# Performance work log

Measured on AMD Instinct MI355X. Metric: run time of the kernel, lower is better.

The kernel has to match this reference:

```python
import jax, jax.numpy as jnp
import numpy as np

B, C, H, W = 16, 256, 32, 32
N_E, E_DIM = 8192, 256
BETA = 0.25
ENT_RATIO = 0.1
TEMP = 0.01


def _normalize(x, eps=1e-6):
    # torch F.normalize: x / clamp_min(||x||, eps)
    n = jnp.linalg.norm(x, axis=-1, keepdims=True)
    return x / jnp.maximum(n, eps)


def setup_inputs() -> dict:
    key = jax.random.key(0)
    k1, k2, k3 = jax.random.split(key, 3)
    z = jax.random.normal(k1, (B, C, H, W), dtype=jnp.float32)
    # nn.Embedding init: normal(0, e_dim**-0.5)
    emb_weight = jax.random.normal(k2, (N_E, E_DIM), dtype=jnp.float32) * (E_DIM ** -0.5)
    # nn.Linear(e_dim, e_dim)
    proj_w = jax.random.normal(k3, (E_DIM, E_DIM), dtype=jnp.float32) * (E_DIM ** -0.5)
    proj_b = jnp.zeros((E_DIM,), dtype=jnp.float32)
    return {"z": z, "emb_weight": emb_weight, "proj_w": proj_w, "proj_b": proj_b}


def reference(z, emb_weight, proj_w, proj_b):
    sg = jax.lax.stop_gradient
    # SimVQ: project the (frozen) codebook through a linear layer
    weight = emb_weight @ proj_w.T + proj_b            # [K, d]
    b, c, h, w = z.shape
    z_bhwc = jnp.transpose(z, (0, 2, 3, 1))            # [B,H,W,C]
    z_flat = z_bhwc.reshape(b, h * w, c)               # [B,L,C]

    # l2_norm=True branch
    zn = _normalize(z_flat)                             # [B,L,d]
    wn = _normalize(weight)                             # [K,d]

    z2 = jnp.sum(zn * zn, axis=-1, keepdims=True)       # [B,L,1]
    w2 = jnp.sum(wn * wn, axis=-1)[None, None, :]       # [1,1,K]
    dot = jnp.einsum('bld,kd->blk', zn, wn)             # [B,L,K]
    dists = z2 + w2 - 2.0 * dot                         # [B,L,K]

    indices = jnp.argmin(dists, axis=-1)                # [B,L]
    q = wn[indices].reshape(b, h, w, c)                 # gather normalized codebook

    # training losses (l2_norm=True -> compare normalized)
    z_cmp = _normalize(z_bhwc)
    q_cmp = _normalize(q)
    codebook_loss = jnp.mean((q_cmp - sg(z_cmp)) ** 2)
    commit_loss = BETA * jnp.mean((sg(q_cmp) - z_cmp) ** 2)

    # entropy loss on affinity = -dists
    a = (-dists).reshape(-1, dists.shape[-1]) / TEMP    # [B*L, K]
    probs = jax.nn.softmax(a, axis=-1)
    log_probs = jax.nn.log_softmax(a + 1e-5, axis=-1)
    avg_probs = jnp.mean(probs, axis=0)
    avg_entropy = -jnp.sum(avg_probs * jnp.log(avg_probs + 1e-5))
    sample_entropy = -jnp.mean(jnp.sum(probs * log_probs, axis=-1))
    entropy_loss = ENT_RATIO * (sample_entropy - avg_entropy)

    # straight-through estimator, back to channel-first
    z_q = z_bhwc + sg(q - z_bhwc)
    z_q = jnp.transpose(z_q, (0, 3, 1, 2))              # [B,C,H,W]
    flat_indices = indices.reshape(-1)
    return (z_q, codebook_loss, commit_loss, entropy_loss, flat_indices)
```

## Files before the change

### kernel.cpp

```cpp
#include <hip/hip_runtime.h>
#include <math.h>

#define NROWS 16384
#define NCODES 8192
#define DIMS 256
#define NCS 4
#define CEXP 288.5390082f

#define OFF_WN   0u
#define OFF_W2   2097152u
#define OFF_ZN   2105344u
#define OFF_WNH  6299648u
#define OFF_WNL  7348224u
#define OFF_ZNH  8396800u
#define OFF_ZNL  10493952u
#define OFF_PL1  12591104u
#define OFF_PL2  12656640u
#define OFF_PS   12722176u
#define OFF_PI1  12787712u
#define OFF_PI2  12853248u
#define OFF_RM   12918784u
#define OFF_RS   12935168u
#define OFF_RIDX 12951552u
#define OFF_AVGP 12967936u
#define OFF_SCAL 12976128u

typedef __attribute__((ext_vector_type(8))) short bf16x8;
typedef __attribute__((ext_vector_type(4))) float f32x4;
typedef unsigned short u16;

__device__ __forceinline__ u16 f2bf(float f) {
  unsigned u = __float_as_uint(f);
  u += 0x7fffu + ((u >> 16) & 1u);
  return (u16)(u >> 16);
}
__device__ __forceinline__ float bf2f(u16 s) { return __uint_as_float(((unsigned)s) << 16); }

__device__ __forceinline__ void gl_lds16(const u16* g, u16* l) {
  __builtin_amdgcn_global_load_lds(
      (const __attribute__((address_space(1))) unsigned*)g,
      (__attribute__((address_space(3))) unsigned*)l, 16, 0, 0);
}

#define PHASE_BARRIER_CNT()  asm volatile("s_waitcnt vmcnt(2) lgkmcnt(0)\n\ts_barrier" ::: "memory")
#define PHASE_BARRIER_ALL()  asm volatile("s_waitcnt vmcnt(0) lgkmcnt(0)\n\ts_barrier" ::: "memory")
#define LGKM_BARRIER()       asm volatile("s_waitcnt lgkmcnt(0)\n\ts_barrier" ::: "memory")
#define DRAIN_VM()           asm volatile("s_waitcnt vmcnt(0)" ::: "memory")

__device__ __forceinline__ void ins2(float x, int idx, float& b1, int& i1, float& b2, int& i2) {
  if (x > b1 || (x == b1 && idx < i1)) { b2 = b1; i2 = i1; b1 = x; i1 = idx; }
  else if (x > b2 || (x == b2 && idx < i2)) { b2 = x; i2 = idx; }
}

__global__ __launch_bounds__(256) void k0_init(float* ws) {
  int i = blockIdx.x * 256 + threadIdx.x;
  if (i < NCODES) ws[OFF_AVGP + i] = 0.f;
  if (i < 16) ws[OFF_SCAL + i] = 0.f;
}

__global__ __launch_bounds__(256) void k1_codebook(const float* __restrict__ emb,
    const float* __restrict__ pw, const float* __restrict__ pb,
    float* __restrict__ wn, float* __restrict__ w2,
    u16* __restrict__ wnh, u16* __restrict__ wnl) {
  __shared__ float e[256];
  __shared__ float red[256];
  int k = blockIdx.x, t = threadIdx.x;
  e[t] = emb[(size_t)k * 256 + t];
  __syncthreads();
  const float4* prow = reinterpret_cast<const float4*>(pw + (size_t)t * 256);
  float acc = pb[t];
  #pragma unroll 8
  for (int q = 0; q < 64; ++q) {
    float4 p4 = prow[q];
    acc += e[q*4+0]*p4.x + e[q*4+1]*p4.y + e[q*4+2]*p4.z + e[q*4+3]*p4.w;
  }
  red[t] = acc * acc;
  __syncthreads();
  for (int s = 128; s; s >>= 1) { if (t < s) red[t] += red[t+s]; __syncthreads(); }
  float inv = 1.f / fmaxf(sqrtf(red[0]), 1e-6f);
  float v = acc * inv;
  size_t o = (size_t)k*256 + t;
  wn[o] = v;
  u16 hb = f2bf(v); float hf = bf2f(hb);
  wnh[o] = hb; wnl[o] = f2bf(v - hf);
  __syncthreads();
  red[t] = v * v;
  __syncthreads();
  for (int s = 128; s; s >>= 1) { if (t < s) red[t] += red[t+s]; __syncthreads(); }
  if (t == 0) w2[k] = red[0];
}

__global__ __launch_bounds__(256) void k2_zn(const float* __restrict__ z,
    float* __restrict__ zn, u16* __restrict__ znh, u16* __restrict__ znl) {
  __shared__ float tile[256][33];
  __shared__ float inv[32];
  int bh = blockIdx.x, t = threadIdx.x;
  const float* zb = z + (size_t)(bh >> 5) * (256*1024) + (size_t)(bh & 31) * 32;
  for (int j = 0; j < 32; ++j) {
    int i = t + j*256; int c = i >> 5, w = i & 31;
    tile[c][w] = zb[(size_t)c*1024 + w];
  }
  __syncthreads();
  if (t < 32) {
    float s = 0.f;
    for (int c = 0; c < 256; ++c) { float v = tile[c][t]; s += v*v; }
    inv[t] = 1.f / fmaxf(sqrtf(s), 1e-6f);
  }
  __syncthreads();
  size_t base = (size_t)bh * 32 * 256;
  for (int w = 0; w < 32; ++w) {
    float v = tile[t][w] * inv[w];
    size_t o = base + (size_t)w*256 + t;
    zn[o] = v;
    u16 hb = f2bf(v); float hf = bf2f(hb);
    znh[o] = hb; znl[o] = f2bf(v - hf);
  }
}

__global__ __attribute__((amdgpu_flat_work_group_size(512,512)))
__attribute__((amdgpu_waves_per_eu(2,4))) void k3_pass1(
    const u16* __restrict__ znh, const u16* __restrict__ znl,
    const u16* __restrict__ wnh, const u16* __restrict__ wnl,
    float* __restrict__ pL1, float* __restrict__ pL2, float* __restrict__ pS,
    int* __restrict__ pI1, int* __restrict__ pI2) {
  __shared__ u16 Cbuf[3][2][128*32];
  __shared__ float mrgF[4][2][32][3];
  __shared__ int   mrgI[4][2][32][2];
  int t = threadIdx.x;
  int rb = blockIdx.x >> 2, cs = blockIdx.x & 3;
  int r0 = rb * 128;
  int w = t >> 6, l = t & 63;
  int wxc = w & 1, wy = w >> 1;
  int g = l >> 4, lr = l & 15;

  bf16x8 bh[2][8], bl[2][8];
  #pragma unroll
  for (int jr = 0; jr < 2; ++jr) {
    size_t rbase = (size_t)(r0 + wy*32 + jr*16 + lr) * 256;
    #pragma unroll
    for (int dc = 0; dc < 8; ++dc) {
      bh[jr][dc] = *(const bf16x8*)&znh[rbase + dc*32 + g*8];
      bl[jr][dc] = *(const bf16x8*)&znl[rbase + dc*32 + g*8];
    }
  }

  const size_t csbase = (size_t)cs * 2048 * 256;
  auto stage = [&](int s, int b) {
    int dc2 = s & 7;
    int krow = (s >> 3) * 128;
    int code = t >> 2, q = t & 3;
    size_t go = csbase + (size_t)(krow + code)*256 + dc2*32 + q*8;
    gl_lds16(&wnh[go], &Cbuf[b][0][w*512]);
    gl_lds16(&wnl[go], &Cbuf[b][1][w*512]);
  };
  DRAIN_VM();
  stage(0, 0);
  stage(1, 1);

  float b1[2] = {-3.0e38f, -3.0e38f}, b2[2] = {-3.0e38f, -3.0e38f}, Sv[2] = {0.f, 0.f};
  int i1[2] = {0, 0}, i2[2] = {0, 0};

  for (int kt = 0; kt < 16; ++kt) {
    f32x4 acc[4][2];
    #pragma unroll
    for (int i = 0; i < 4; ++i) { acc[i][0] = (f32x4){0.f,0.f,0.f,0.f}; acc[i][1] = (f32x4){0.f,0.f,0.f,0.f}; }
    #pragma unroll
    for (int dc = 0; dc < 8; ++dc) {
      int s = kt*8 + dc;
      if (s < 127) PHASE_BARRIER_CNT(); else PHASE_BARRIER_ALL();
      if (s + 2 < 128) {
        int bS = s + 2; bS -= (bS/3)*3;
        stage(s + 2, bS);
      }
      int bR = s - (s/3)*3;
      #pragma unroll
      for (int i = 0; i < 4; ++i) {
        int co = (wxc*64 + i*16 + lr)*32 + g*8;
        bf16x8 ah = *(const bf16x8*)&Cbuf[bR][0][co];
        bf16x8 al = *(const bf16x8*)&Cbuf[bR][1][co];
        acc[i][0] = __builtin_amdgcn_mfma_f32_16x16x32_bf16(ah, bh[0][dc], acc[i][0], 0, 0, 0);
        acc[i][1] = __builtin_amdgcn_mfma_f32_16x16x32_bf16(ah, bh[1][dc], acc[i][1], 0, 0, 0);
        acc[i][0] = __builtin_amdgcn_mfma_f32_16x16x32_bf16(ah, bl[0][dc], acc[i][0], 0, 0, 0);
        acc[i][1] = __builtin_amdgcn_mfma_f32_16x16x32_bf16(ah, bl[1][dc], acc[i][1], 0, 0, 0);
        acc[i][0] = __builtin_amdgcn_mfma_f32_16x16x32_bf16(al, bh[0][dc], acc[i][0], 0, 0, 0);
        acc[i][1] = __builtin_amdgcn_mfma_f32_16x16x32_bf16(al, bh[1][dc], acc[i][1], 0, 0, 0);
      }
    }
    int kb16 = kt * 16;
    #pragma unroll
    for (int jr = 0; jr < 2; ++jr) {
      float xv[16];
      #pragma unroll
      for (int n = 0; n < 16; ++n) xv[n] = acc[n>>2][jr][n&3];
      float ob1 = b1[jr];
      #pragma unroll
      for (int n = 0; n < 16; ++n) {
        float x = xv[n];
        bool c1 = x > b1[jr];
        bool c2 = x > b2[jr];
        float hi = fmaxf(x, b1[jr]);
        float lo = fminf(x, b1[jr]);
        b2[jr] = fmaxf(lo, fminf(hi, b2[jr]));
        i2[jr] = c1 ? i1[jr] : (c2 ? (kb16 + n) : i2[jr]);
        b1[jr] = hi;
        i1[jr] = c1 ? (kb16 + n) : i1[jr];
      }
      float negCm = -CEXP * b1[jr];
      float ts0 = 0.f, ts1 = 0.f;
      #pragma unroll
      for (int n = 0; n < 16; n += 2) {
        ts0 += exp2f(fmaf(CEXP, xv[n],   negCm));
        ts1 += exp2f(fmaf(CEXP, xv[n+1], negCm));
      }
      Sv[jr] = Sv[jr] * exp2f(CEXP * (ob1 - b1[jr])) + (ts0 + ts1);
    }
  }
  float my[2], y2[2]; int gi1[2], gi2[2];
  #pragma unroll
  for (int jr = 0; jr < 2; ++jr) {
    int e1 = i1[jr], e2 = i2[jr];
    int base = cs*2048 + wxc*64 + g*4;
    gi1[jr] = base + (e1>>4)*128 + ((e1&15)>>2)*16 + (e1&3);
    gi2[jr] = base + (e2>>4)*128 + ((e2&15)>>2)*16 + (e2&3);
    my[jr] = CEXP * b1[jr];
    y2[jr] = CEXP * b2[jr];
    #pragma unroll
    for (int mask = 16; mask <= 32; mask <<= 1) {
      float om  = __shfl_xor(my[jr], mask, 64);
      float oy2 = __shfl_xor(y2[jr], mask, 64);
      float oS  = __shfl_xor(Sv[jr], mask, 64);
      int   o1  = __shfl_xor(gi1[jr], mask, 64);
      int   o2  = __shfl_xor(gi2[jr], mask, 64);
      float pm = my[jr];
      ins2(om,  o1, my[jr], gi1[jr], y2[jr], gi2[jr]);
      ins2(oy2, o2, my[jr], gi1[jr], y2[jr], gi2[jr]);
      Sv[jr] = Sv[jr] * exp2f(pm - my[jr]) + oS * exp2f(om - my[jr]);
    }
  }
  __syncthreads();
  if (g == 0) {
    #pragma unroll
    for (int jr = 0; jr < 2; ++jr) {
      int ri = jr*16 + lr;
      mrgF[wy][wxc][ri][0] = my[jr]; mrgF[wy][wxc][ri][1] = y2[jr]; mrgF[wy][wxc][ri][2] = Sv[jr];
      mrgI[wy][wxc][ri][0] = gi1[jr]; mrgI[wy][wxc][ri][1] = gi2[jr];
    }
  }
  __syncthreads();
  if (t < 128) {
    int wyy = t >> 5, ri = t & 31;
    float m1 = mrgF[wyy][0][ri][0], m2 = mrgF[wyy][0][ri][1], S = mrgF[wyy][0][ri][2];
    int a1 = mrgI[wyy][0][ri][0], a2 = mrgI[wyy][0][ri][1];
    float om1 = mrgF[wyy][1][ri][0], om2 = mrgF[wyy][1][ri][1], oS = mrgF[wyy][1][ri][2];
    int ob1i = mrgI[wyy][1][ri][0], ob2i = mrgI[wyy][1][ri][1];
    float pm = m1;
    ins2(om1, ob1i, m1, a1, m2, a2);
    ins2(om2, ob2i, m1, a1, m2, a2);
    S = S * exp2f(pm - m1) + oS * exp2f(om1 - m1);
    int r = r0 + wyy*32 + ri;
    size_t o = (size_t)cs * NROWS + r;
    pL1[o] = m1; pL2[o] = m2; pS[o] = S;
    pI1[o] = a1; pI2[o] = a2;
  }
}

__global__ __launch_bounds__(256) void k3b_refine(
    const float* __restrict__ zn, const float* __restrict__ wn, const float* __restrict__ w2,
    const float* __restrict__ pL1, const float* __restrict__ pL2, const float* __restrict__ pS,
    const int* __restrict__ pI1, const int* __restrict__ pI2,
    float* __restrict__ rm, float* __restrict__ rs, int* __restrict__ ridx) {
  int t = threadIdx.x;
  int r = blockIdx.x * 4 + (t >> 6);
  int l = t & 63;
  float b1 = pL1[r], b2 = pL2[r], S = pS[r];
  int i1 = pI1[r], i2 = pI2[r];
  #pragma unroll
  for (int c = 1; c < NCS; ++c) {
    size_t o = (size_t)c * NROWS + r;
    float ob1 = pL1[o], ob2 = pL2[o], oS = pS[o];
    int oi1 = pI1[o], oi2 = pI2[o];
    float pb1 = b1;
    ins2(ob1, oi1, b1, i1, b2, i2);
    ins2(ob2, oi2, b1, i1, b2, i2);
    S = S * exp2f(pb1 - b1) + oS * exp2f(ob1 - b1);
  }
  int cand = (l < 32) ? i1 : i2;
  int lo = l & 31;
  const float* zr = zn + (size_t)r * 256;
  const float* wc = wn + (size_t)cand * 256;
  float d = 0.f;
  #pragma unroll
  for (int q = 0; q < 8; ++q) d += zr[lo + q*32] * wc[lo + q*32];
  #pragma unroll
  for (int mask = 1; mask <= 16; mask <<= 1) d += __shfl_xor(d, mask, 64);
  float dOther = __shfl_xor(d, 32, 64);
  if (l == 0) {
    float s1 = w2[i1] - 2.f*d;
    float s2 = w2[i2] - 2.f*dOther;
    int win = i1;
    if (s2 < s1 || (s2 == s1 && i2 < i1)) win = i2;
    rm[r] = b1; rs[r] = S; ridx[r] = win;
  }
}

__global__ __attribute__((amdgpu_flat_work_group_size(512,512)))
__attribute__((amdgpu_waves_per_eu(2,4))) void k4_pass2(
    const u16* __restrict__ znh, const u16* __restrict__ znl,
    const u16* __restrict__ wnh, const u16* __restrict__ wnl,
    const float* __restrict__ rm, const float* __restrict__ rs,
    float* __restrict__ avgp, float* __restrict__ scal) {
  __shared__ u16 Cbuf[3][2][128*32];
  __shared__ float avgLds[4][128];
  __shared__ float red[512];
  int t = threadIdx.x;
  int rb = blockIdx.x >> 2, cs = blockIdx.x & 3;
  int r0 = rb * 128;
  int w = t >> 6, l = t & 63;
  int wxc = w & 1, wy = w >> 1;
  int g = l >> 4, lr = l & 15;

  bf16x8 bh[2][8], bl[2][8];
  #pragma unroll
  for (int jr = 0; jr < 2; ++jr) {
    size_t rbase = (size_t)(r0 + wy*32 + jr*16 + lr) * 256;
    #pragma unroll
    for (int dc = 0; dc < 8; ++dc) {
      bh[jr][dc] = *(const bf16x8*)&znh[rbase + dc*32 + g*8];
      bl[jr][dc] = *(const bf16x8*)&znl[rbase + dc*32 + g*8];
    }
  }
  float m_[2], invS[2], l2s[2];
  #pragma unroll
  for (int jr = 0; jr < 2; ++jr) {
    int r = r0 + wy*32 + jr*16 + lr;
    float mm = rm[r], ss = rs[r];
    m_[jr] = mm; invS[jr] = 1.f / ss; l2s[jr] = log2f(ss);
  }

  const size_t csbase = (size_t)cs * 2048 * 256;
  auto stage = [&](int s, int b) {
    int dc2 = s & 7;
    int krow = (s >> 3) * 128;
    int code = t >> 2, q = t & 3;
    size_t go = csbase + (size_t)(krow + code)*256 + dc2*32 + q*8;
    gl_lds16(&wnh[go], &Cbuf[b][0][w*512]);
    gl_lds16(&wnl[go], &Cbuf[b][1][w*512]);
  };
  DRAIN_VM();
  stage(0, 0);
  stage(1, 1);
  float ent = 0.f;

  for (int kt = 0; kt < 16; ++kt) {
    f32x4 acc[4][2];
    #pragma unroll
    for (int i = 0; i < 4; ++i) { acc[i][0] = (f32x4){0.f,0.f,0.f,0.f}; acc[i][1] = (f32x4){0.f,0.f,0.f,0.f}; }
    #pragma unroll
    for (int dc = 0; dc < 8; ++dc) {
      int s = kt*8 + dc;
      if (s < 127) PHASE_BARRIER_CNT(); else PHASE_BARRIER_ALL();
      if (s + 2 < 128) {
        int bS = s + 2; bS -= (bS/3)*3;
        stage(s + 2, bS);
      }
      int bR = s - (s/3)*3;
      #pragma unroll
      for (int i = 0; i < 4; ++i) {
        int co = (wxc*64 + i*16 + lr)*32 + g*8;
        bf16x8 ah = *(const bf16x8*)&Cbuf[bR][0][co];
        bf16x8 al = *(const bf16x8*)&Cbuf[bR][1][co];
        acc[i][0] = __builtin_amdgcn_mfma_f32_16x16x32_bf16(ah, bh[0][dc], acc[i][0], 0, 0, 0);
        acc[i][1] = __builtin_amdgcn_mfma_f32_16x16x32_bf16(ah, bh[1][dc], acc[i][1], 0, 0, 0);
        acc[i][0] = __builtin_amdgcn_mfma_f32_16x16x32_bf16(ah, bl[0][dc], acc[i][0], 0, 0, 0);
        acc[i][1] = __builtin_amdgcn_mfma_f32_16x16x32_bf16(ah, bl[1][dc], acc[i][1], 0, 0, 0);
        acc[i][0] = __builtin_amdgcn_mfma_f32_16x16x32_bf16(al, bh[0][dc], acc[i][0], 0, 0, 0);
        acc[i][1] = __builtin_amdgcn_mfma_f32_16x16x32_bf16(al, bh[1][dc], acc[i][1], 0, 0, 0);
      }
    }
    int kb = cs*2048 + kt*128;
    float codeAcc[16];
    #pragma unroll
    for (int n = 0; n < 16; ++n) codeAcc[n] = 0.f;
    #pragma unroll
    for (int jr = 0; jr < 2; ++jr) {
      float m = m_[jr], is = invS[jr], l2 = l2s[jr];
      #pragma unroll
      for (int i = 0; i < 4; ++i)
        #pragma unroll
        for (int v = 0; v < 4; ++v) {
          float tt = fmaf(CEXP, acc[i][jr][v], -m);
          float p = exp2f(tt) * is;
          ent -= p * (tt - l2);
          codeAcc[i*4+v] += p;
        }
    }
    #pragma unroll
    for (int n = 0; n < 16; ++n) {
      float s = codeAcc[n];
      s += __shfl_xor(s, 1, 64);
      s += __shfl_xor(s, 2, 64);
      s += __shfl_xor(s, 4, 64);
      s += __shfl_xor(s, 8, 64);
      if (lr == 0) avgLds[wy][wxc*64 + (n>>2)*16 + g*4 + (n&3)] = s;
    }
    LGKM_BARRIER();
    if (t < 128) atomicAdd(&avgp[kb + t],
        (avgLds[0][t] + avgLds[1][t] + avgLds[2][t] + avgLds[3][t]) * (1.f/16384.f));
  }
  red[t] = ent;
  __syncthreads();
  for (int s2 = 256; s2; s2 >>= 1) { if (t < s2) red[t] += red[t + s2]; __syncthreads(); }
  if (t == 0) atomicAdd(&scal[1], red[0] * 0.6931471806f);
}

__global__ __launch_bounds__(256) void k5_gather(const float* __restrict__ zn,
    const float* __restrict__ wn, const int* __restrict__ row_idx,
    float* __restrict__ out_zq, float* __restrict__ scal) {
  __shared__ float tile[256][33];
  __shared__ float red4[4];
  __shared__ float red[256];
  int bh = blockIdx.x, t = threadIdx.x;
  int b = bh >> 5, h = bh & 31;
  float cb = 0.f;
  for (int w = 0; w < 32; ++w) {
    int r = bh*32 + w;
    int idx = row_idx[r];
    float q = wn[(size_t)idx*256 + t];
    float s = q*q;
    #pragma unroll
    for (int mask = 32; mask; mask >>= 1) s += __shfl_xor(s, mask, 64);
    if ((t & 63) == 0) red4[t >> 6] = s;
    __syncthreads();
    float tot = red4[0] + red4[1] + red4[2] + red4[3];
    float inv = 1.f / fmaxf(sqrtf(tot), 1e-6f);
    float zv = zn[(size_t)r*256 + t];
    float d = q*inv - zv;
    cb += d*d;
    tile[t][w] = q;
    __syncthreads();
  }
  red[t] = cb;
  __syncthreads();
  for (int s2 = 128; s2; s2 >>= 1) { if (t < s2) red[t] += red[t+s2]; __syncthreads(); }
  if (t == 0) atomicAdd(&scal[0], red[0]);
  float* ob = out_zq + (size_t)b*256*1024 + (size_t)h*32;
  for (int j = 0; j < 32; ++j) {
    int i = t + j*256; int c = i >> 5, ww = i & 31;
    ob[(size_t)c*1024 + ww] = tile[c][ww];
  }
}

__global__ __launch_bounds__(256) void k6_final(const float* __restrict__ avg_probs,
    const float* __restrict__ scal, const int* __restrict__ row_idx,
    float* __restrict__ out) {
  int t = threadIdx.x;
  if (blockIdx.x < 64) {
    int r = blockIdx.x*256 + t;
    out[4194307 + r] = (float)row_idx[r];
    return;
  }
  __shared__ float red[256];
  float s = 0.f;
  for (int j = 0; j < 32; ++j) {
    float v = avg_probs[t + j*256];
    s -= v * logf(v + 1e-5f);
  }
  red[t] = s;
  __syncthreads();
  for (int q = 128; q; q >>= 1) { if (t < q) red[t] += red[t+q]; __syncthreads(); }
  if (t == 0) {
    float avg_entropy = red[0];
    float sample_entropy = scal[1] * (1.f/16384.f);
    float cb = scal[0] * (1.f/4194304.f);
    out[4194304] = cb;
    out[4194305] = 0.25f * cb;
    out[4194306] = 0.1f * (sample_entropy - avg_entropy);
  }
}

extern "C" void kernel_launch(void* const* d_in, const int* in_sizes, int n_in,
                              void* d_out, int out_size, void* d_ws, size_t ws_size,
                              hipStream_t stream) {
  const float* z   = (const float*)d_in[0];
  const float* emb = (const float*)d_in[1];
  const float* pw  = (const float*)d_in[2];
  const float* pb  = (const float*)d_in[3];
  float* ws  = (float*)d_ws;
  float* out = (float*)d_out;
  float* wn   = ws + OFF_WN;
  float* w2   = ws + OFF_W2;
  float* zn   = ws + OFF_ZN;
  u16*   wnh  = (u16*)(ws + OFF_WNH);
  u16*   wnl  = (u16*)(ws + OFF_WNL);
  u16*   znh  = (u16*)(ws + OFF_ZNH);
  u16*   znl  = (u16*)(ws + OFF_ZNL);
  float* pL1  = ws + OFF_PL1;
  float* pL2  = ws + OFF_PL2;
  float* pS   = ws + OFF_PS;
  int*   pI1  = (int*)(ws + OFF_PI1);
  int*   pI2  = (int*)(ws + OFF_PI2);
  float* rm   = ws + OFF_RM;
  float* rs   = ws + OFF_RS;
  int*   ridx = (int*)(ws + OFF_RIDX);
  float* avgp = ws + OFF_AVGP;
  float* scal = ws + OFF_SCAL;

  k0_init<<<32, 256, 0, stream>>>(ws);
  k1_codebook<<<NCODES, 256, 0, stream>>>(emb, pw, pb, wn, w2, wnh, wnl);
  k2_zn<<<512, 256, 0, stream>>>(z, zn, znh, znl);
  k3_pass1<<<512, 512, 0, stream>>>(znh, znl, wnh, wnl, pL1, pL2, pS, pI1, pI2);
  k3b_refine<<<NROWS/4, 256, 0, stream>>>(zn, wn, w2, pL1, pL2, pS, pI1, pI2, rm, rs, ridx);
  k4_pass2<<<512, 512, 0, stream>>>(znh, znl, wnh, wnl, rm, rs, avgp, scal);
  k5_gather<<<512, 256, 0, stream>>>(zn, wn, ridx, out, scal);
  k6_final<<<65, 256, 0, stream>>>(avgp, scal, ridx, out);
}
```

Measured before the change: 866.9 us.

## Give each wave all 128 codes per tile and 256 rows per block

Both GEMM passes now have each wave compute all 128 staged codes against its own 32 rows, so a block covers 256 rows and the grid is halved. This doubles reuse of each staged codebook tile and removes the cross-wave LDS merge and its barriers in pass 1. Pass 2 accumulates per-code probabilities in a block-local LDS slice with shared atomics and flushes to global once at the end, replacing the per-tile barrier plus global atomics. The cost is twice the accumulator registers (waves_per_eu is pinned to 2), only 256 blocks in flight, and contention on the LDS atomics.

Result: faster. 792.9 us (-8.5%).

```diff
diff --git a/kernel.cpp b/kernel.cpp
--- a/kernel.cpp
+++ b/kernel.cpp
@@ -44,7 +44,6 @@
 
 #define PHASE_BARRIER_CNT()  asm volatile("s_waitcnt vmcnt(2) lgkmcnt(0)\n\ts_barrier" ::: "memory")
 #define PHASE_BARRIER_ALL()  asm volatile("s_waitcnt vmcnt(0) lgkmcnt(0)\n\ts_barrier" ::: "memory")
-#define LGKM_BARRIER()       asm volatile("s_waitcnt lgkmcnt(0)\n\ts_barrier" ::: "memory")
 #define DRAIN_VM()           asm volatile("s_waitcnt vmcnt(0)" ::: "memory")
 
 __device__ __forceinline__ void ins2(float x, int idx, float& b1, int& i1, float& b2, int& i2) {
@@ -118,25 +117,22 @@
 }
 
 __global__ __attribute__((amdgpu_flat_work_group_size(512,512)))
-__attribute__((amdgpu_waves_per_eu(2,4))) void k3_pass1(
+__attribute__((amdgpu_waves_per_eu(2,2))) void k3_pass1(
     const u16* __restrict__ znh, const u16* __restrict__ znl,
     const u16* __restrict__ wnh, const u16* __restrict__ wnl,
     float* __restrict__ pL1, float* __restrict__ pL2, float* __restrict__ pS,
     int* __restrict__ pI1, int* __restrict__ pI2) {
   __shared__ u16 Cbuf[3][2][128*32];
-  __shared__ float mrgF[4][2][32][3];
-  __shared__ int   mrgI[4][2][32][2];
   int t = threadIdx.x;
   int rb = blockIdx.x >> 2, cs = blockIdx.x & 3;
-  int r0 = rb * 128;
+  int r0 = rb * 256;
   int w = t >> 6, l = t & 63;
-  int wxc = w & 1, wy = w >> 1;
   int g = l >> 4, lr = l & 15;
 
   bf16x8 bh[2][8], bl[2][8];
   #pragma unroll
   for (int jr = 0; jr < 2; ++jr) {
-    size_t rbase = (size_t)(r0 + wy*32 + jr*16 + lr) * 256;
+    size_t rbase = (size_t)(r0 + w*32 + jr*16 + lr) * 256;
     #pragma unroll
     for (int dc = 0; dc < 8; ++dc) {
       bh[jr][dc] = *(const bf16x8*)&znh[rbase + dc*32 + g*8];
@@ -148,8 +144,8 @@
   auto stage = [&](int s, int b) {
     int dc2 = s & 7;
     int krow = (s >> 3) * 128;
-    int code = t >> 2, q = t & 3;
-    size_t go = csbase + (size_t)(krow + code)*256 + dc2*32 + q*8;
+    int c = w*16 + (l >> 2), q = l & 3;
+    size_t go = csbase + (size_t)(krow + c)*256 + dc2*32 + q*8;
     gl_lds16(&wnh[go], &Cbuf[b][0][w*512]);
     gl_lds16(&wnl[go], &Cbuf[b][1][w*512]);
   };
@@ -161,9 +157,9 @@
   int i1[2] = {0, 0}, i2[2] = {0, 0};
 
   for (int kt = 0; kt < 16; ++kt) {
-    f32x4 acc[4][2];
-    #pragma unroll
-    for (int i = 0; i < 4; ++i) { acc[i][0] = (f32x4){0.f,0.f,0.f,0.f}; acc[i][1] = (f32x4){0.f,0.f,0.f,0.f}; }
+    f32x4 acc[8][2];
+    #pragma unroll
+    for (int i = 0; i < 8; ++i) { acc[i][0] = (f32x4){0.f,0.f,0.f,0.f}; acc[i][1] = (f32x4){0.f,0.f,0.f,0.f}; }
     #pragma unroll
     for (int dc = 0; dc < 8; ++dc) {
       int s = kt*8 + dc;
@@ -174,8 +170,8 @@
       }
       int bR = s - (s/3)*3;
       #pragma unroll
-      for (int i = 0; i < 4; ++i) {
-        int co = (wxc*64 + i*16 + lr)*32 + g*8;
+      for (int i = 0; i < 8; ++i) {
+        int co = (i*16 + lr)*32 + g*8;
         bf16x8 ah = *(const bf16x8*)&Cbuf[bR][0][co];
         bf16x8 al = *(const bf16x8*)&Cbuf[bR][1][co];
         acc[i][0] = __builtin_amdgcn_mfma_f32_16x16x32_bf16(ah, bh[0][dc], acc[i][0], 0, 0, 0);
@@ -186,31 +182,28 @@
         acc[i][1] = __builtin_amdgcn_mfma_f32_16x16x32_bf16(al, bh[1][dc], acc[i][1], 0, 0, 0);
       }
     }
-    int kb16 = kt * 16;
+    int kb32 = kt * 32;
     #pragma unroll
     for (int jr = 0; jr < 2; ++jr) {
-      float xv[16];
-      #pragma unroll
-      for (int n = 0; n < 16; ++n) xv[n] = acc[n>>2][jr][n&3];
       float ob1 = b1[jr];
       #pragma unroll
-      for (int n = 0; n < 16; ++n) {
-        float x = xv[n];
+      for (int n = 0; n < 32; ++n) {
+        float x = acc[n>>2][jr][n&3];
         bool c1 = x > b1[jr];
         bool c2 = x > b2[jr];
         float hi = fmaxf(x, b1[jr]);
         float lo = fminf(x, b1[jr]);
         b2[jr] = fmaxf(lo, fminf(hi, b2[jr]));
-        i2[jr] = c1 ? i1[jr] : (c2 ? (kb16 + n) : i2[jr]);
+        i2[jr] = c1 ? i1[jr] : (c2 ? (kb32 + n) : i2[jr]);
         b1[jr] = hi;
-        i1[jr] = c1 ? (kb16 + n) : i1[jr];
+        i1[jr] = c1 ? (kb32 + n) : i1[jr];
       }
       float negCm = -CEXP * b1[jr];
       float ts0 = 0.f, ts1 = 0.f;
       #pragma unroll
-      for (int n = 0; n < 16; n += 2) {
-        ts0 += exp2f(fmaf(CEXP, xv[n],   negCm));
-        ts1 += exp2f(fmaf(CEXP, xv[n+1], negCm));
+      for (int n = 0; n < 32; n += 2) {
+        ts0 += exp2f(fmaf(CEXP, acc[n>>2][jr][n&3],     negCm));
+        ts1 += exp2f(fmaf(CEXP, acc[(n+1)>>2][jr][(n+1)&3], negCm));
       }
       Sv[jr] = Sv[jr] * exp2f(CEXP * (ob1 - b1[jr])) + (ts0 + ts1);
     }
@@ -219,9 +212,9 @@
   #pragma unroll
   for (int jr = 0; jr < 2; ++jr) {
     int e1 = i1[jr], e2 = i2[jr];
-    int base = cs*2048 + wxc*64 + g*4;
-    gi1[jr] = base + (e1>>4)*128 + ((e1&15)>>2)*16 + (e1&3);
-    gi2[jr] = base + (e2>>4)*128 + ((e2&15)>>2)*16 + (e2&3);
+    int base = cs*2048 + g*4;
+    gi1[jr] = base + (e1>>5)*128 + ((e1>>2)&7)*16 + (e1&3);
+    gi2[jr] = base + (e2>>5)*128 + ((e2>>2)&7)*16 + (e2&3);
     my[jr] = CEXP * b1[jr];
     y2[jr] = CEXP * b2[jr];
     #pragma unroll
@@ -237,30 +230,14 @@
       Sv[jr] = Sv[jr] * exp2f(pm - my[jr]) + oS * exp2f(om - my[jr]);
     }
   }
-  __syncthreads();
   if (g == 0) {
     #pragma unroll
     for (int jr = 0; jr < 2; ++jr) {
-      int ri = jr*16 + lr;
-      mrgF[wy][wxc][ri][0] = my[jr]; mrgF[wy][wxc][ri][1] = y2[jr]; mrgF[wy][wxc][ri][2] = Sv[jr];
-      mrgI[wy][wxc][ri][0] = gi1[jr]; mrgI[wy][wxc][ri][1] = gi2[jr];
-    }
-  }
-  __syncthreads();
-  if (t < 128) {
-    int wyy = t >> 5, ri = t & 31;
-    float m1 = mrgF[wyy][0][ri][0], m2 = mrgF[wyy][0][ri][1], S = mrgF[wyy][0][ri][2];
-    int a1 = mrgI[wyy][0][ri][0], a2 = mrgI[wyy][0][ri][1];
-    float om1 = mrgF[wyy][1][ri][0], om2 = mrgF[wyy][1][ri][1], oS = mrgF[wyy][1][ri][2];
-    int ob1i = mrgI[wyy][1][ri][0], ob2i = mrgI[wyy][1][ri][1];
-    float pm = m1;
-    ins2(om1, ob1i, m1, a1, m2, a2);
-    ins2(om2, ob2i, m1, a1, m2, a2);
-    S = S * exp2f(pm - m1) + oS * exp2f(om1 - m1);
-    int r = r0 + wyy*32 + ri;
-    size_t o = (size_t)cs * NROWS + r;
-    pL1[o] = m1; pL2[o] = m2; pS[o] = S;
-    pI1[o] = a1; pI2[o] = a2;
+      int r = r0 + w*32 + jr*16 + lr;
+      size_t o = (size_t)cs * NROWS + r;
+      pL1[o] = my[jr]; pL2[o] = y2[jr]; pS[o] = Sv[jr];
+      pI1[o] = gi1[jr]; pI2[o] = gi2[jr];
+    }
   }
 }
 
@@ -304,25 +281,26 @@
 }
 
 __global__ __attribute__((amdgpu_flat_work_group_size(512,512)))
-__attribute__((amdgpu_waves_per_eu(2,4))) void k4_pass2(
+__attribute__((amdgpu_waves_per_eu(2,2))) void k4_pass2(
     const u16* __restrict__ znh, const u16* __restrict__ znl,
     const u16* __restrict__ wnh, const u16* __restrict__ wnl,
     const float* __restrict__ rm, const float* __restrict__ rs,
     float* __restrict__ avgp, float* __restrict__ scal) {
   __shared__ u16 Cbuf[3][2][128*32];
-  __shared__ float avgLds[4][128];
+  __shared__ float avgSlice[2048];
   __shared__ float red[512];
   int t = threadIdx.x;
   int rb = blockIdx.x >> 2, cs = blockIdx.x & 3;
-  int r0 = rb * 128;
+  int r0 = rb * 256;
   int w = t >> 6, l = t & 63;
-  int wxc = w & 1, wy = w >> 1;
   int g = l >> 4, lr = l & 15;
 
+  for (int i = t; i < 2048; i += 512) avgSlice[i] = 0.f;
+
   bf16x8 bh[2][8], bl[2][8];
   #pragma unroll
   for (int jr = 0; jr < 2; ++jr) {
-    size_t rbase = (size_t)(r0 + wy*32 + jr*16 + lr) * 256;
+    size_t rbase = (size_t)(r0 + w*32 + jr*16 + lr) * 256;
     #pragma unroll
     for (int dc = 0; dc < 8; ++dc) {
       bh[jr][dc] = *(const bf16x8*)&znh[rbase + dc*32 + g*8];
@@ -332,7 +310,7 @@
   float m_[2], invS[2], l2s[2];
   #pragma unroll
   for (int jr = 0; jr < 2; ++jr) {
-    int r = r0 + wy*32 + jr*16 + lr;
+    int r = r0 + w*32 + jr*16 + lr;
     float mm = rm[r], ss = rs[r];
     m_[jr] = mm; invS[jr] = 1.f / ss; l2s[jr] = log2f(ss);
   }
@@ -341,8 +319,8 @@
   auto stage = [&](int s, int b) {
     int dc2 = s & 7;
     int krow = (s >> 3) * 128;
-    int code = t >> 2, q = t & 3;
-    size_t go = csbase + (size_t)(krow + code)*256 + dc2*32 + q*8;
+    int c = w*16 + (l >> 2), q = l & 3;
+    size_t go = csbase + (size_t)(krow + c)*256 + dc2*32 + q*8;
     gl_lds16(&wnh[go], &Cbuf[b][0][w*512]);
     gl_lds16(&wnl[go], &Cbuf[b][1][w*512]);
   };
@@ -352,9 +330,9 @@
   float ent = 0.f;
 
   for (int kt = 0; kt < 16; ++kt) {
-    f32x4 acc[4][2];
-    #pragma unroll
-    for (int i = 0; i < 4; ++i) { acc[i][0] = (f32x4){0.f,0.f,0.f,0.f}; acc[i][1] = (f32x4){0.f,0.f,0.f,0.f}; }
+    f32x4 acc[8][2];
+    #pragma unroll
+    for (int i = 0; i < 8; ++i) { acc[i][0] = (f32x4){0.f,0.f,0.f,0.f}; acc[i][1] = (f32x4){0.f,0.f,0.f,0.f}; }
     #pragma unroll
     for (int dc = 0; dc < 8; ++dc) {
       int s = kt*8 + dc;
@@ -365,8 +343,8 @@
       }
       int bR = s - (s/3)*3;
       #pragma unroll
-      for (int i = 0; i < 4; ++i) {
-        int co = (wxc*64 + i*16 + lr)*32 + g*8;
+      for (int i = 0; i < 8; ++i) {
+        int co = (i*16 + lr)*32 + g*8;
         bf16x8 ah = *(const bf16x8*)&Cbuf[bR][0][co];
         bf16x8 al = *(const bf16x8*)&Cbuf[bR][1][co];
         acc[i][0] = __builtin_amdgcn_mfma_f32_16x16x32_bf16(ah, bh[0][dc], acc[i][0], 0, 0, 0);
@@ -377,36 +355,41 @@
         acc[i][1] = __builtin_amdgcn_mfma_f32_16x16x32_bf16(al, bh[1][dc], acc[i][1], 0, 0, 0);
       }
     }
-    int kb = cs*2048 + kt*128;
-    float codeAcc[16];
-    #pragma unroll
-    for (int n = 0; n < 16; ++n) codeAcc[n] = 0.f;
-    #pragma unroll
-    for (int jr = 0; jr < 2; ++jr) {
-      float m = m_[jr], is = invS[jr], l2 = l2s[jr];
-      #pragma unroll
-      for (int i = 0; i < 4; ++i)
+    #pragma unroll
+    for (int half = 0; half < 2; ++half) {
+      float ca[16];
+      #pragma unroll
+      for (int n = 0; n < 16; ++n) ca[n] = 0.f;
+      #pragma unroll
+      for (int jr = 0; jr < 2; ++jr) {
+        float m = m_[jr], is = invS[jr], l2 = l2s[jr];
         #pragma unroll
-        for (int v = 0; v < 4; ++v) {
-          float tt = fmaf(CEXP, acc[i][jr][v], -m);
-          float p = exp2f(tt) * is;
-          ent -= p * (tt - l2);
-          codeAcc[i*4+v] += p;
+        for (int ii = 0; ii < 4; ++ii) {
+          int i = half*4 + ii;
+          #pragma unroll
+          for (int v = 0; v < 4; ++v) {
+            float tt = fmaf(CEXP, acc[i][jr][v], -m_[jr]);
+            float p = exp2f(tt) * is;
+            ent -= p * (tt - l2);
+            ca[ii*4+v] += p;
+          }
         }
-    }
-    #pragma unroll
-    for (int n = 0; n < 16; ++n) {
-      float s = codeAcc[n];
-      s += __shfl_xor(s, 1, 64);
-      s += __shfl_xor(s, 2, 64);
-      s += __shfl_xor(s, 4, 64);
-      s += __shfl_xor(s, 8, 64);
-      if (lr == 0) avgLds[wy][wxc*64 + (n>>2)*16 + g*4 + (n&3)] = s;
-    }
-    LGKM_BARRIER();
-    if (t < 128) atomicAdd(&avgp[kb + t],
-        (avgLds[0][t] + avgLds[1][t] + avgLds[2][t] + avgLds[3][t]) * (1.f/16384.f));
-  }
+      }
+      #pragma unroll
+      for (int n = 0; n < 16; ++n) {
+        float sv = ca[n];
+        sv += __shfl_xor(sv, 1, 64);
+        sv += __shfl_xor(sv, 2, 64);
+        sv += __shfl_xor(sv, 4, 64);
+        sv += __shfl_xor(sv, 8, 64);
+        if (lr == 0)
+          atomicAdd(&avgSlice[kt*128 + (half*4 + (n>>2))*16 + g*4 + (n&3)], sv);
+      }
+    }
+  }
+  __syncthreads();
+  for (int i = t; i < 2048; i += 512)
+    atomicAdd(&avgp[cs*2048 + i], avgSlice[i] * (1.f/16384.f));
   red[t] = ent;
   __syncthreads();
   for (int s2 = 256; s2; s2 >>= 1) { if (t < s2) red[t] += red[t + s2]; __syncthreads(); }
@@ -508,9 +491,9 @@
   k0_init<<<32, 256, 0, stream>>>(ws);
   k1_codebook<<<NCODES, 256, 0, stream>>>(emb, pw, pb, wn, w2, wnh, wnl);
   k2_zn<<<512, 256, 0, stream>>>(z, zn, znh, znl);
-  k3_pass1<<<512, 512, 0, stream>>>(znh, znl, wnh, wnl, pL1, pL2, pS, pI1, pI2);
+  k3_pass1<<<256, 512, 0, stream>>>(znh, znl, wnh, wnl, pL1, pL2, pS, pI1, pI2);
   k3b_refine<<<NROWS/4, 256, 0, stream>>>(zn, wn, w2, pL1, pL2, pS, pI1, pI2, rm, rs, ridx);
-  k4_pass2<<<512, 512, 0, stream>>>(znh, znl, wnh, wnl, rm, rs, avgp, scal);
+  k4_pass2<<<256, 512, 0, stream>>>(znh, znl, wnh, wnl, rm, rs, avgp, scal);
   k5_gather<<<512, 256, 0, stream>>>(zn, wn, ridx, out, scal);
   k6_final<<<65, 256, 0, stream>>>(avgp, scal, ridx, out);
 }
```
